# Kernel tuning notes

Measured on AMD Instinct MI355X. Metric: run time of the kernel, lower is better.

Reference implementation:

```python
import jax, jax.numpy as jnp
import numpy as np

BETA = 0.25
SK_EPSILONS = [0.0, 0.0, 0.003]
SK_ITERS = 50
B_SIZE = 262144
LATENT_DIM = 32
K = 256


def setup_inputs() -> dict:
    key = jax.random.key(0)
    kz, k0, k1, k2 = jax.random.split(key, 4)
    return {
        "z": jax.random.normal(kz, (B_SIZE, LATENT_DIM), dtype=jnp.float32),
        "cb0": jax.random.normal(k0, (K, LATENT_DIM), dtype=jnp.float32),
        "cb1": jax.random.normal(k1, (K, LATENT_DIM), dtype=jnp.float32),
        "cb2": jax.random.normal(k2, (K, LATENT_DIM), dtype=jnp.float32),
    }


def _sq_dists(residual, codebook):
    # ||r - c||^2 = ||r||^2 + ||c||^2 - 2 r.c  -> (B, K), avoids (B,K,D) broadcast
    r2 = jnp.sum(residual * residual, axis=1, keepdims=True)      # (B,1)
    c2 = jnp.sum(codebook * codebook, axis=1)                     # (K,)
    cross = residual @ codebook.T                                 # (B,K)
    return r2 + c2 - 2.0 * cross


def _sinkhorn(d_centered, epsilon, n_iters):
    # log-domain Sinkhorn-Knopp, matches torch reference
    B, Kk = d_centered.shape
    log_B = jnp.log(jnp.asarray(B, dtype=d_centered.dtype))
    log_K = jnp.log(jnp.asarray(Kk, dtype=d_centered.dtype))
    log_Q = -d_centered / epsilon
    log_Q = log_Q - jax.scipy.special.logsumexp(log_Q)

    def body(_, lq):
        lq = lq - jax.scipy.special.logsumexp(lq, axis=1, keepdims=True) - log_B
        lq = lq - jax.scipy.special.logsumexp(lq, axis=0, keepdims=True) - log_K
        return lq

    log_Q = jax.lax.fori_loop(0, n_iters, body, log_Q)
    return jnp.exp(log_Q + log_B)


def _quantize_level(residual, codebook, sk_epsilon, use_sk=True):
    dists = _sq_dists(residual, codebook)  # (B, K)
    codes_argmin = jnp.argmin(dists, axis=-1)
    if use_sk and sk_epsilon > 0:
        d = jax.lax.stop_gradient(dists)
        d_max = jnp.max(d)
        d_min = jnp.min(d)
        mid = (d_max + d_min) / 2
        amp = jnp.maximum(d_max - mid, 1e-05)
        Q = _sinkhorn((d - mid) / amp, sk_epsilon, SK_ITERS)
        bad = jnp.any(jnp.isnan(Q)) | jnp.any(jnp.isinf(Q))
        codes = jnp.where(bad, codes_argmin, jnp.argmax(Q, axis=-1))
    else:
        codes = codes_argmin
    quantized = codebook[codes]  # (B, D) gather
    return codes, quantized


def reference(z, cb0, cb1, cb2):
    codebooks = [cb0, cb1, cb2]
    sg = jax.lax.stop_gradient
    residual = z
    all_codes = []
    quantized_total = jnp.zeros_like(z)
    rq_loss = jnp.asarray(0.0, dtype=z.dtype)
    for codebook, sk_epsilon in zip(codebooks, SK_EPSILONS):
        codes, e = _quantize_level(residual, codebook, sk_epsilon, use_sk=True)
        all_codes.append(codes)
        rq_loss = rq_loss + jnp.mean((sg(residual) - e) ** 2)
        rq_loss = rq_loss + BETA * jnp.mean((residual - sg(e)) ** 2)
        e_st = residual + sg(e - residual)  # straight-through
        quantized_total = quantized_total + e_st
        residual = residual - sg(e)
    return (all_codes[0], all_codes[1], all_codes[2], quantized_total, rq_loss)
```

## Files before the change

kernel.cpp:

```cpp
#include <hip/hip_runtime.h>


#define BSZ   262144
#define DIM   32
#define KK    256
#define CHUNK 128
#define NBLK  (BSZ / CHUNK)
#define ITBLK 256
#define NIBLK (BSZ / ITBLK)
#define LROW  36
#define SKEPS 0.003f
#define NIT   50

#define WS_SSQ  0
#define WS_MINK 1
#define WS_MAXK 2
#define WS_TWOT 3
#define WS_W0   256
#define WS_WA   512
#define WS_SIGB 4096
#define WS_BHU  8192
#define WS_BLU  12288

#define OC0   0
#define OC1   BSZ
#define OC2   (2 * BSZ)
#define OQ    (3 * BSZ)
#define OLOSS (3 * BSZ + BSZ * DIM)
#define OU_AH (3u * BSZ)
#define OU_AL (3u * BSZ + 4194304u)

typedef _Float16 half8 __attribute__((ext_vector_type(8)));
typedef float f32x4 __attribute__((ext_vector_type(4)));

#if __has_builtin(__builtin_amdgcn_exp2f)
#define EXP2(x) __builtin_amdgcn_exp2f(x)
#else
#define EXP2(x) exp2f(x)
#endif

#if __has_builtin(__builtin_amdgcn_update_dpp)
#define ROR16(x, N)                                                            \
  __int_as_float(__builtin_amdgcn_update_dpp(__float_as_int(x),                \
                 __float_as_int(x), 0x120 + (N), 0xF, 0xF, false))
#else
#define ROR16(x, N) __shfl_xor((x), (N))
#endif

__device__ __forceinline__ float wred_max(float x) {
  x = fmaxf(x, ROR16(x, 1)); x = fmaxf(x, ROR16(x, 2));
  x = fmaxf(x, ROR16(x, 4)); x = fmaxf(x, ROR16(x, 8));
  x = fmaxf(x, __shfl_xor(x, 16)); x = fmaxf(x, __shfl_xor(x, 32));
  return x;
}
__device__ __forceinline__ float wred_min(float x) {
  x = fminf(x, ROR16(x, 1)); x = fminf(x, ROR16(x, 2));
  x = fminf(x, ROR16(x, 4)); x = fminf(x, ROR16(x, 8));
  x = fminf(x, __shfl_xor(x, 16)); x = fminf(x, __shfl_xor(x, 32));
  return x;
}
__device__ __forceinline__ float wred_sum(float x) {
  x += ROR16(x, 1); x += ROR16(x, 2); x += ROR16(x, 4); x += ROR16(x, 8);
  x += __shfl_xor(x, 16); x += __shfl_xor(x, 32);
  return x;
}
__device__ __forceinline__ float g16_max(float x) {
  x = fmaxf(x, ROR16(x, 1)); x = fmaxf(x, ROR16(x, 2));
  x = fmaxf(x, ROR16(x, 4)); x = fmaxf(x, ROR16(x, 8));
  return x;
}
__device__ __forceinline__ float g16_sum(float x) {
  x += ROR16(x, 1); x += ROR16(x, 2); x += ROR16(x, 4); x += ROR16(x, 8);
  return x;
}

__device__ __forceinline__ unsigned fkey(float f) {
  unsigned b = __float_as_uint(f);
  return (b & 0x80000000u) ? ~b : (b | 0x80000000u);
}
__device__ __forceinline__ float fkeyinv(unsigned k) {
  return __uint_as_float((k & 0x80000000u) ? (k ^ 0x80000000u) : ~k);
}
__device__ __forceinline__ unsigned pk2h(_Float16 a, _Float16 b) {
  unsigned short ua = __builtin_bit_cast(unsigned short, a);
  unsigned short ub = __builtin_bit_cast(unsigned short, b);
  return (unsigned)ua | ((unsigned)ub << 16);
}

__device__ __forceinline__ void load_cbregs_pin(const float* __restrict__ cb, int lane,
                                                float scale, float cbr[4][DIM]) {
#pragma unroll
  for (int c = 0; c < 4; ++c) {
    const float4* p = reinterpret_cast<const float4*>(cb + (4 * lane + c) * DIM);
#pragma unroll
    for (int k = 0; k < 8; ++k) {
      float4 v = p[k];
      cbr[c][4 * k + 0] = v.x * scale; cbr[c][4 * k + 1] = v.y * scale;
      cbr[c][4 * k + 2] = v.z * scale; cbr[c][4 * k + 3] = v.w * scale;
    }
  }
}
__device__ __forceinline__ void cb_norms(const float cbr[4][DIM], float c2[4]) {
#pragma unroll
  for (int c = 0; c < 4; ++c) {
    float s = 0.f;
#pragma unroll
    for (int i = 0; i < DIM; ++i) s = fmaf(cbr[c][i], cbr[c][i], s);
    c2[c] = s;
  }
}
__device__ __forceinline__ void dot4x4(const float* zr, const float cbr[4][DIM],
                                       float v[4][4]) {
#pragma unroll
  for (int d = 0; d < DIM; d += 4) {
#pragma unroll
    for (int q = 0; q < 4; ++q) {
      float4 a = *reinterpret_cast<const float4*>(zr + q * LROW + d);
#pragma unroll
      for (int c = 0; c < 4; ++c) {
        v[q][c] = fmaf(cbr[c][d + 0], a.x, v[q][c]);
        v[q][c] = fmaf(cbr[c][d + 1], a.y, v[q][c]);
        v[q][c] = fmaf(cbr[c][d + 2], a.z, v[q][c]);
        v[q][c] = fmaf(cbr[c][d + 3], a.w, v[q][c]);
      }
    }
  }
}

__global__ void init_k(unsigned* __restrict__ wsu, unsigned long long* __restrict__ sig0) {
  sig0[threadIdx.x] = 0ull;
  if (threadIdx.x == 0) {
    wsu[WS_SSQ] = 0u; wsu[WS_MINK] = 0xFFFFFFFFu; wsu[WS_MAXK] = 0u;
  }
}

__device__ __forceinline__ void argmin_phase(const float* __restrict__ cb, const float* zl,
                                             const float* rsq, int* codel, int lane, int wid) {
  float cbr[4][DIM], c2[4];
  load_cbregs_pin(cb, lane, 1.0f, cbr);
  cb_norms(cbr, c2);
  for (int rb = 0; rb < 8; ++rb) {
    const int r0 = wid * 32 + rb * 4;
    float v[4][4];
#pragma unroll
    for (int q = 0; q < 4; ++q) { v[q][0] = 0.f; v[q][1] = 0.f; v[q][2] = 0.f; v[q][3] = 0.f; }
    dot4x4(&zl[r0 * LROW], cbr, v);
    float d0[4], d1[4], d2[4], d3[4], bq[4], mq[4];
#pragma unroll
    for (int q = 0; q < 4; ++q) {
      float r2 = rsq[r0 + q];
      d0[q] = fmaf(-2.f, v[q][0], r2 + c2[0]);
      d1[q] = fmaf(-2.f, v[q][1], r2 + c2[1]);
      d2[q] = fmaf(-2.f, v[q][2], r2 + c2[2]);
      d3[q] = fmaf(-2.f, v[q][3], r2 + c2[3]);
      bq[q] = fminf(fminf(d0[q], d1[q]), fminf(d2[q], d3[q]));
    }
#pragma unroll
    for (int q = 0; q < 4; ++q) mq[q] = wred_min(bq[q]);
#pragma unroll
    for (int q = 0; q < 4; ++q) {
      int cbi = (d0[q] == mq[q]) ? 0 : ((d1[q] == mq[q]) ? 1 : ((d2[q] == mq[q]) ? 2 : 3));
      unsigned long long bl = __ballot(bq[q] == mq[q]);
      int src = __ffsll(bl) - 1;
      int code = __shfl(4 * lane + cbi, src);
      if (lane == 0) codel[r0 + q] = code;
    }
  }
}

__device__ __forceinline__ void remap_phase(const float* __restrict__ cb, float* zl,
                                            float* rsq, const int* codel, int tid) {
  int row = tid & (CHUNK - 1);
  int half = tid >> 7;
  const float4* cbg = reinterpret_cast<const float4*>(cb + codel[row] * DIM + half * 16);
  float4* zr = reinterpret_cast<float4*>(&zl[row * LROW + half * 16]);
  float local = 0.f;
#pragma unroll
  for (int k = 0; k < 4; ++k) {
    float4 cv = cbg[k];
    float4 v = zr[k];
    v.x -= cv.x; v.y -= cv.y; v.z -= cv.z; v.w -= cv.w;
    zr[k] = v;
    local = fmaf(v.x, v.x, local); local = fmaf(v.y, v.y, local);
    local = fmaf(v.z, v.z, local); local = fmaf(v.w, v.w, local);
  }
  atomicAdd(&rsq[row], local);
}

__global__ __launch_bounds__(256, 2) void stageA_k(const float* __restrict__ z,
                                                   const float* __restrict__ cb0,
                                                   const float* __restrict__ cb1,
                                                   const float* __restrict__ cb2,
                                                   float* __restrict__ out,
                                                   unsigned* __restrict__ outu,
                                                   unsigned* __restrict__ wsu,
                                                   float* __restrict__ wsf) {
  __shared__ float zl[CHUNK * LROW];
  __shared__ float rsq[CHUNK];
  __shared__ int codel[CHUNK];
  __shared__ float red[4];
  const int tid = threadIdx.x, lane = tid & 63, wid = tid >> 6;
  const long base = (long)blockIdx.x * CHUNK;

#pragma unroll
  for (int g = 0; g < 4; ++g) {
    int f4 = g * 256 + tid;
    float4 v = reinterpret_cast<const float4*>(z + base * DIM)[f4];
    int row = f4 >> 3, d = (f4 & 7) * 4;
    *reinterpret_cast<float4*>(&zl[row * LROW + d]) = v;
  }
  __syncthreads();
  if (tid < CHUNK) {
    float s = 0.f;
#pragma unroll
    for (int d = 0; d < DIM; ++d) { float x = zl[tid * LROW + d]; s = fmaf(x, x, s); }
    rsq[tid] = s;
  }
  __syncthreads();

  float loss_acc = 0.f;

  argmin_phase(cb0, zl, rsq, codel, lane, wid);
  __syncthreads();
  if (tid < CHUNK) { out[OC0 + base + tid] = (float)codel[tid]; rsq[tid] = 0.f; }
  __syncthreads();
  remap_phase(cb0, zl, rsq, codel, tid);
  __syncthreads();
  if (tid < CHUNK) loss_acc += rsq[tid];

  argmin_phase(cb1, zl, rsq, codel, lane, wid);
  __syncthreads();
  if (tid < CHUNK) { out[OC1 + base + tid] = (float)codel[tid]; rsq[tid] = 0.f; }
  __syncthreads();
  remap_phase(cb1, zl, rsq, codel, tid);
  __syncthreads();
  if (tid < CHUNK) loss_acc += rsq[tid];

#pragma unroll
  for (int g2 = 0; g2 < 8; ++g2) {
    int slot = g2 * 256 + tid;
    int b = slot >> 8;
    int l = (slot >> 2) & 63;
    int u = slot & 3;
    int row = b * 16 + (l & 15);
    int k = (l >> 4) * 8 + u * 2;
    float x0 = zl[row * LROW + k], x1 = zl[row * LROW + k + 1];
    _Float16 h0 = (_Float16)x0, h1 = (_Float16)x1;
    _Float16 q0 = (_Float16)(x0 - (float)h0), q1 = (_Float16)(x1 - (float)h1);
    unsigned gbase = ((unsigned)blockIdx.x * 8u + (unsigned)b) * 256u + (unsigned)(l * 4 + u);
    outu[OU_AH + gbase] = pk2h(h0, h1);
    outu[OU_AL + gbase] = pk2h(q0, q1);
  }

  {
    float cbr[4][DIM], c2[4];
    load_cbregs_pin(cb2, lane, 1.0f, cbr);
    cb_norms(cbr, c2);
    float dmn = 3.4e38f, dmx = -3.4e38f;
    for (int rb = 0; rb < 8; ++rb) {
      const int r0 = wid * 32 + rb * 4;
      float v[4][4];
#pragma unroll
      for (int q = 0; q < 4; ++q) { v[q][0] = 0.f; v[q][1] = 0.f; v[q][2] = 0.f; v[q][3] = 0.f; }
      dot4x4(&zl[r0 * LROW], cbr, v);
#pragma unroll
      for (int q = 0; q < 4; ++q) {
        float r2 = rsq[r0 + q];
#pragma unroll
        for (int c = 0; c < 4; ++c) {
          float dd = fmaf(-2.f, v[q][c], r2 + c2[c]);
          dmn = fminf(dmn, dd); dmx = fmaxf(dmx, dd);
        }
      }
    }
    dmn = wred_min(dmn);
    dmx = wred_max(dmx);
    if (lane == 0) {
      atomicMin(&wsu[WS_MINK], fkey(dmn));
      atomicMax(&wsu[WS_MAXK], fkey(dmx));
    }
  }

  loss_acc = wred_sum(loss_acc);
  if (lane == 0) red[wid] = loss_acc;
  __syncthreads();
  if (tid == 0) atomicAdd(&wsf[WS_SSQ], red[0] + red[1] + red[2] + red[3]);
}

__global__ void prep_k(const float* __restrict__ cb2, unsigned* __restrict__ wsu,
                       float* __restrict__ wsf, unsigned* __restrict__ bh,
                       unsigned* __restrict__ bl) {
  int j = threadIdx.x;
  float dmin = fkeyinv(wsu[WS_MINK]);
  float dmax = fkeyinv(wsu[WS_MAXK]);
  float mid = (dmax + dmin) * 0.5f;
  float amp = fmaxf(dmax - mid, 1e-5f);
  float t = 1.0f / (amp * SKEPS);
  const float L2E = 1.4426950408889634f;
  float T2L = 2.0f * t * L2E;
  if (j == 0) wsf[WS_TWOT] = T2L;
  float s = 0.f;
#pragma unroll
  for (int d = 0; d < DIM; ++d) { float c = cb2[j * DIM + d]; s = fmaf(c, c, s); }
  wsf[WS_W0 + j] = -t * L2E * s;
  for (int g = 0; g < 16; ++g) {
    int slot = g * 256 + j;
    int jt = slot >> 8, l = (slot >> 2) & 63, u = slot & 3;
    int col = jt * 16 + (l & 15);
    int k = (l >> 4) * 8 + u * 2;
    float b0 = T2L * cb2[col * DIM + k], b1 = T2L * cb2[col * DIM + k + 1];
    _Float16 h0 = (_Float16)b0, h1 = (_Float16)b1;
    _Float16 q0 = (_Float16)(b0 - (float)h0), q1 = (_Float16)(b1 - (float)h1);
    bh[slot] = pk2h(h0, h1);
    bl[slot] = pk2h(q0, q1);
  }
}

__global__ __launch_bounds__(256, 2) void iter_k(const uint4* __restrict__ afh,
                                                 const uint4* __restrict__ afl,
                                                 const uint4* __restrict__ bfh,
                                                 const uint4* __restrict__ bfl,
                                                 const float* __restrict__ w_rd,
                                                 float* __restrict__ w_wr,
                                                 const unsigned long long* __restrict__ s_rd,
                                                 unsigned long long* __restrict__ s_wr,
                                                 unsigned long long* __restrict__ s_zr,
                                                 int first) {
  __shared__ float wsh[KK];
  __shared__ float exm[8][2][2][16];
  __shared__ float exs[8][2][2][16];
  __shared__ float ssh[2][KK];
  const int tid = threadIdx.x, lane = tid & 63, wv = tid >> 6;
  const int pair = wv >> 1, ch = wv & 1, g = lane >> 4;

  {
    float wj = first ? w_rd[tid]
                     : w_rd[tid] + 34.0f - log2f(fmaxf((float)s_rd[tid], 1.0f));
    wsh[tid] = wj;
    if (blockIdx.x == 0) { w_wr[tid] = wj; s_zr[tid] = 0ull; }
  }
  half8 Bh[8], Bl[8];
#pragma unroll
  for (int jt = 0; jt < 8; ++jt) {
    Bh[jt] = __builtin_bit_cast(half8, bfh[(ch * 8 + jt) * 64 + lane]);
    Bl[jt] = __builtin_bit_cast(half8, bfl[(ch * 8 + jt) * 64 + lane]);
  }
  __syncthreads();
  float wc[8];
#pragma unroll
  for (int jt = 0; jt < 8; ++jt) wc[jt] = wsh[(ch * 8 + jt) * 16 + (lane & 15)];

  float sg[8] = {0.f, 0.f, 0.f, 0.f, 0.f, 0.f, 0.f, 0.f};

  for (int b = 0; b < 8; ++b) {
    const int batchid = blockIdx.x * 16 + pair * 8 + b;
    half8 Ah = __builtin_bit_cast(half8, afh[batchid * 64 + lane]);
    half8 Al = __builtin_bit_cast(half8, afl[batchid * 64 + lane]);
    f32x4 v[8];
#pragma unroll
    for (int jt = 0; jt < 8; ++jt) {
      f32x4 acc = {0.f, 0.f, 0.f, 0.f};
      acc = __builtin_amdgcn_mfma_f32_16x16x32_f16(Al, Bl[jt], acc, 0, 0, 0);
      acc = __builtin_amdgcn_mfma_f32_16x16x32_f16(Al, Bh[jt], acc, 0, 0, 0);
      acc = __builtin_amdgcn_mfma_f32_16x16x32_f16(Ah, Bl[jt], acc, 0, 0, 0);
      acc = __builtin_amdgcn_mfma_f32_16x16x32_f16(Ah, Bh[jt], acc, 0, 0, 0);
      v[jt] = acc;
    }
    float m[4];
#pragma unroll
    for (int r = 0; r < 4; ++r) {
#pragma unroll
      for (int jt = 0; jt < 8; ++jt) v[jt][r] += wc[jt];
      float a01 = fmaxf(v[0][r], v[1][r]), a23 = fmaxf(v[2][r], v[3][r]);
      float a45 = fmaxf(v[4][r], v[5][r]), a67 = fmaxf(v[6][r], v[7][r]);
      m[r] = g16_max(fmaxf(fmaxf(a01, a23), fmaxf(a45, a67)));
    }
    float s[4];
#pragma unroll
    for (int r = 0; r < 4; ++r) {
#pragma unroll
      for (int jt = 0; jt < 8; ++jt) v[jt][r] = EXP2(v[jt][r] - m[r]);
      float s01 = v[0][r] + v[1][r], s23 = v[2][r] + v[3][r];
      float s45 = v[4][r] + v[5][r], s67 = v[6][r] + v[7][r];
      s[r] = g16_sum((s01 + s23) + (s45 + s67));
    }
    if ((lane & 15) == 0) {
      *reinterpret_cast<float4*>(&exm[b][pair][ch][g * 4]) = make_float4(m[0], m[1], m[2], m[3]);
      *reinterpret_cast<float4*>(&exs[b][pair][ch][g * 4]) = make_float4(s[0], s[1], s[2], s[3]);
    }
    __syncthreads();
    float4 pm = *reinterpret_cast<const float4*>(&exm[b][pair][ch ^ 1][g * 4]);
    float4 ps = *reinterpret_cast<const float4*>(&exs[b][pair][ch ^ 1][g * 4]);
    float rinv[4];
    {
      float pmv[4] = {pm.x, pm.y, pm.z, pm.w};
      float psv[4] = {ps.x, ps.y, ps.z, ps.w};
#pragma unroll
      for (int r = 0; r < 4; ++r) {
        float M = fmaxf(m[r], pmv[r]);
        float sc = EXP2(m[r] - M);
        float tot = fmaf(s[r], sc, psv[r] * EXP2(pmv[r] - M));
        rinv[r] = sc * __builtin_amdgcn_rcpf(tot);
      }
    }
#pragma unroll
    for (int jt = 0; jt < 8; ++jt)
#pragma unroll
      for (int r = 0; r < 4; ++r) sg[jt] = fmaf(v[jt][r], rinv[r], sg[jt]);
  }
#pragma unroll
  for (int jt = 0; jt < 8; ++jt) {
    float x = sg[jt];
    x += __shfl_xor(x, 16); x += __shfl_xor(x, 32);
    sg[jt] = x;
  }
  if (lane < 16) {
#pragma unroll
    for (int jt = 0; jt < 8; ++jt) ssh[pair][ch * 128 + jt * 16 + lane] = sg[jt];
  }
  __syncthreads();
  float stot = ssh[0][tid] + ssh[1][tid];
  atomicAdd(&s_wr[tid], (unsigned long long)fmaf(stot, 16777216.0f, 0.5f));
}

__global__ __launch_bounds__(256, 2) void final_k(const float* __restrict__ z,
                                                  const float* __restrict__ cb0,
                                                  const float* __restrict__ cb1,
                                                  const float* __restrict__ cb2,
                                                  float* __restrict__ out,
                                                  const float* __restrict__ wsf,
                                                  float* __restrict__ wssq,
                                                  const float* __restrict__ w_rd,
                                                  const unsigned long long* __restrict__ s_rd) {
  __shared__ float zl[CHUNK * LROW];
  __shared__ float wsh[KK];
  __shared__ int codel[CHUNK];
  __shared__ float red[4];
  const int tid = threadIdx.x, lane = tid & 63, wid = tid >> 6;
  const long base = (long)blockIdx.x * CHUNK;

  wsh[tid] = w_rd[tid] + 34.0f - log2f(fmaxf((float)s_rd[tid], 1.0f));

#pragma unroll
  for (int g = 0; g < 4; ++g) {
    int f4 = g * 256 + tid;
    float4 vv = reinterpret_cast<const float4*>(z + base * DIM)[f4];
    int row = f4 >> 3, d = (f4 & 7) * 4;
    *reinterpret_cast<float4*>(&zl[row * LROW + d]) = vv;
  }
  __syncthreads();
  {
    int row = tid & (CHUNK - 1);
    int half = tid >> 7;
    int c0 = (int)out[OC0 + base + row];
    int c1 = (int)out[OC1 + base + row];
    const float4* e0 = reinterpret_cast<const float4*>(cb0 + c0 * DIM + half * 16);
    const float4* e1 = reinterpret_cast<const float4*>(cb1 + c1 * DIM + half * 16);
    float4* zr = reinterpret_cast<float4*>(&zl[row * LROW + half * 16]);
#pragma unroll
    for (int k = 0; k < 4; ++k) {
      float4 a = e0[k], bb = e1[k], v = zr[k];
      v.x = (v.x - a.x) - bb.x; v.y = (v.y - a.y) - bb.y;
      v.z = (v.z - a.z) - bb.z; v.w = (v.w - a.w) - bb.w;
      zr[k] = v;
    }
  }
  const float twot = wsf[WS_TWOT];
  float cbr[4][DIM];
  load_cbregs_pin(cb2, lane, twot, cbr);
  __syncthreads();
  float wc[4];
#pragma unroll
  for (int c = 0; c < 4; ++c) wc[c] = wsh[4 * lane + c];

  for (int rb = 0; rb < 8; ++rb) {
    const int r0 = wid * 32 + rb * 4;
    float v[4][4];
#pragma unroll
    for (int q = 0; q < 4; ++q) { v[q][0] = wc[0]; v[q][1] = wc[1]; v[q][2] = wc[2]; v[q][3] = wc[3]; }
    dot4x4(&zl[r0 * LROW], cbr, v);
    float bq[4], mq[4];
#pragma unroll
    for (int q = 0; q < 4; ++q)
      bq[q] = fmaxf(fmaxf(v[q][0], v[q][1]), fmaxf(v[q][2], v[q][3]));
#pragma unroll
    for (int q = 0; q < 4; ++q) mq[q] = wred_max(bq[q]);
#pragma unroll
    for (int q = 0; q < 4; ++q) {
      int cbi = (v[q][0] == mq[q]) ? 0 : ((v[q][1] == mq[q]) ? 1 : ((v[q][2] == mq[q]) ? 2 : 3));
      unsigned long long bl = __ballot(bq[q] == mq[q]);
      int src = __ffsll(bl) - 1;
      int code = __shfl(4 * lane + cbi, src);
      if (lane == 0) codel[r0 + q] = code;
    }
  }
  __syncthreads();
  if (tid < CHUNK) out[OC2 + base + tid] = (float)codel[tid];
  float loss_acc = 0.f;
#pragma unroll
  for (int g = 0; g < 4; ++g) {
    int f4 = g * 256 + tid;
    int row = f4 >> 3, d = (f4 & 7) * 4;
    float4 e = *reinterpret_cast<const float4*>(cb2 + codel[row] * DIM + d);
    float4 r = *reinterpret_cast<const float4*>(&zl[row * LROW + d]);
    float4 zv = reinterpret_cast<const float4*>(z + base * DIM)[f4];
    float4 q;
    q.x = zv.x - r.x + e.x; q.y = zv.y - r.y + e.y;
    q.z = zv.z - r.z + e.z; q.w = zv.w - r.w + e.w;
    reinterpret_cast<float4*>(out + OQ + base * DIM)[f4] = q;
    float rx = r.x - e.x, ry = r.y - e.y, rz = r.z - e.z, rw = r.w - e.w;
    loss_acc = fmaf(rx, rx, loss_acc); loss_acc = fmaf(ry, ry, loss_acc);
    loss_acc = fmaf(rz, rz, loss_acc); loss_acc = fmaf(rw, rw, loss_acc);
  }
  loss_acc = wred_sum(loss_acc);
  if (lane == 0) red[wid] = loss_acc;
  __syncthreads();
  if (tid == 0) atomicAdd(&wssq[WS_SSQ], red[0] + red[1] + red[2] + red[3]);
}

__global__ void losswrite_k(float* __restrict__ out, const float* __restrict__ wsf) {
  if (threadIdx.x == 0) out[OLOSS] = 1.25f * wsf[WS_SSQ] / 8388608.0f;
}

extern "C" void kernel_launch(void* const* d_in, const int* in_sizes, int n_in,
                              void* d_out, int out_size, void* d_ws, size_t ws_size,
                              hipStream_t stream) {
  const float* z   = (const float*)d_in[0];
  const float* cb0 = (const float*)d_in[1];
  const float* cb1 = (const float*)d_in[2];
  const float* cb2 = (const float*)d_in[3];
  float* out = (float*)d_out;
  unsigned* outu = (unsigned*)d_out;
  float* wsf = (float*)d_ws;
  unsigned* wsu = (unsigned*)d_ws;
  unsigned long long* sig = (unsigned long long*)((char*)d_ws + WS_SIGB);
  unsigned* bh = (unsigned*)d_ws + WS_BHU;
  unsigned* bl = (unsigned*)d_ws + WS_BLU;

  const uint4* afh = (const uint4*)(outu + OU_AH);
  const uint4* afl = (const uint4*)(outu + OU_AL);
  const uint4* bfh = (const uint4*)bh;
  const uint4* bfl = (const uint4*)bl;

  init_k<<<1, 256, 0, stream>>>(wsu, sig);
  stageA_k<<<NBLK, 256, 0, stream>>>(z, cb0, cb1, cb2, out, outu, wsu, wsf);
  prep_k<<<1, 256, 0, stream>>>(cb2, wsu, wsf, bh, bl);
  for (int it = 0; it < NIT; ++it) {
    const float* w_rd = (it == 0) ? (wsf + WS_W0) : (wsf + WS_WA + ((it - 1) & 1) * KK);
    float* w_wr = wsf + WS_WA + (it & 1) * KK;
    const unsigned long long* s_rd = sig + KK * ((it + 2) % 3);
    unsigned long long* s_wr = sig + KK * (it % 3);
    unsigned long long* s_zr = sig + KK * ((it + 1) % 3);
    iter_k<<<NIBLK, 256, 0, stream>>>(afh, afl, bfh, bfl, w_rd, w_wr, s_rd, s_wr, s_zr,
                                      it == 0 ? 1 : 0);
  }
  final_k<<<NBLK, 256, 0, stream>>>(z, cb0, cb1, cb2, out, wsf, wsf,
                                    wsf + WS_WA + ((NIT - 1) & 1) * KK,
                                    sig + KK * ((NIT - 1) % 3));
  losswrite_k<<<1, 64, 0, stream>>>(out, wsf);
}
```

Baseline: 2.334 ms.

## Move distance GEMMs to bf16x3 MFMA and split final stage into codes/output kernels

Replaces the scalar FMA dot-product loops for the level-0/1 argmin, the level-2 min/max scan and the final Sinkhorn argmax with MFMA 16x16x32 bf16 instructions. Inputs are split into three bf16 terms and combined with six MFMAs to keep near-fp32 accuracy, using codebook fragments precomputed in a new prep kernel. The iteration kernel is restructured, and the final stage is split into a code-selection kernel and a separate kernel that rebuilds the quantized output and loss from the stored codes. The gain is tensor-core throughput; the costs are the extra split arithmetic, possible argmax tie or rounding differences, and re-reading z and the codes in the new output pass.

```diff
diff --git a/kernel.cpp b/kernel.cpp
--- a/kernel.cpp
+++ b/kernel.cpp
@@ -6,8 +6,7 @@
 #define KK    256
 #define CHUNK 128
 #define NBLK  (BSZ / CHUNK)
-#define ITBLK 256
-#define NIBLK (BSZ / ITBLK)
+#define NIBLK (BSZ / 256)
 #define LROW  36
 #define SKEPS 0.003f
 #define NIT   50
@@ -18,9 +17,11 @@
 #define WS_TWOT 3
 #define WS_W0   256
 #define WS_WA   512
-#define WS_SIGB 4096
-#define WS_BHU  8192
-#define WS_BLU  12288
+#define WS_C2   1024
+#define WSB_SIG 8192
+#define WSB_BH  16384
+#define WSB_BL  32768
+#define WSB_QB  49152
 
 #define OC0   0
 #define OC1   BSZ
@@ -30,6 +31,7 @@
 #define OU_AH (3u * BSZ)
 #define OU_AL (3u * BSZ + 4194304u)
 
+typedef short short8 __attribute__((ext_vector_type(8)));
 typedef _Float16 half8 __attribute__((ext_vector_type(8)));
 typedef float f32x4 __attribute__((ext_vector_type(4)));
 
@@ -43,8 +45,10 @@
 #define ROR16(x, N)                                                            \
   __int_as_float(__builtin_amdgcn_update_dpp(__float_as_int(x),                \
                  __float_as_int(x), 0x120 + (N), 0xF, 0xF, false))
+#define ROR16I(x, N) __builtin_amdgcn_update_dpp((x), (x), 0x120 + (N), 0xF, 0xF, false)
 #else
 #define ROR16(x, N) __shfl_xor((x), (N))
+#define ROR16I(x, N) __shfl_xor((x), (N))
 #endif
 
 __device__ __forceinline__ float wred_max(float x) {
@@ -73,6 +77,12 @@
   x += ROR16(x, 1); x += ROR16(x, 2); x += ROR16(x, 4); x += ROR16(x, 8);
   return x;
 }
+__device__ __forceinline__ void g16_argmax(float& v, int& j) {
+  { float ov = ROR16(v,1); int oj = ROR16I(j,1); if (ov > v || (ov == v && oj < j)) { v = ov; j = oj; } }
+  { float ov = ROR16(v,2); int oj = ROR16I(j,2); if (ov > v || (ov == v && oj < j)) { v = ov; j = oj; } }
+  { float ov = ROR16(v,4); int oj = ROR16I(j,4); if (ov > v || (ov == v && oj < j)) { v = ov; j = oj; } }
+  { float ov = ROR16(v,8); int oj = ROR16I(j,8); if (ov > v || (ov == v && oj < j)) { v = ov; j = oj; } }
+}
 
 __device__ __forceinline__ unsigned fkey(float f) {
   unsigned b = __float_as_uint(f);
@@ -86,90 +96,115 @@
   unsigned short ub = __builtin_bit_cast(unsigned short, b);
   return (unsigned)ua | ((unsigned)ub << 16);
 }
-
-__device__ __forceinline__ void load_cbregs_pin(const float* __restrict__ cb, int lane,
-                                                float scale, float cbr[4][DIM]) {
-#pragma unroll
-  for (int c = 0; c < 4; ++c) {
-    const float4* p = reinterpret_cast<const float4*>(cb + (4 * lane + c) * DIM);
-#pragma unroll
-    for (int k = 0; k < 8; ++k) {
-      float4 v = p[k];
-      cbr[c][4 * k + 0] = v.x * scale; cbr[c][4 * k + 1] = v.y * scale;
-      cbr[c][4 * k + 2] = v.z * scale; cbr[c][4 * k + 3] = v.w * scale;
-    }
-  }
-}
-__device__ __forceinline__ void cb_norms(const float cbr[4][DIM], float c2[4]) {
-#pragma unroll
-  for (int c = 0; c < 4; ++c) {
+__device__ __forceinline__ unsigned short bf16rne(float x) {
+  unsigned u = __float_as_uint(x);
+  return (unsigned short)((u + 0x7FFFu + ((u >> 16) & 1u)) >> 16);
+}
+__device__ __forceinline__ float bf2f(unsigned short h) {
+  return __uint_as_float(((unsigned)h) << 16);
+}
+__device__ __forceinline__ void split3_8(const float* xs, short8& a1, short8& a2, short8& a3) {
+#pragma unroll
+  for (int u = 0; u < 8; ++u) {
+    float x = xs[u];
+    unsigned short b1 = bf16rne(x); x -= bf2f(b1);
+    unsigned short b2 = bf16rne(x); x -= bf2f(b2);
+    unsigned short b3 = bf16rne(x);
+    a1[u] = (short)b1; a2[u] = (short)b2; a3[u] = (short)b3;
+  }
+}
+__device__ __forceinline__ f32x4 mfma6(short8 A1, short8 A2, short8 A3,
+                                       const uint4* __restrict__ q1,
+                                       const uint4* __restrict__ q2,
+                                       const uint4* __restrict__ q3,
+                                       int idx, f32x4 acc) {
+  short8 B1 = __builtin_bit_cast(short8, q1[idx]);
+  short8 B2 = __builtin_bit_cast(short8, q2[idx]);
+  short8 B3 = __builtin_bit_cast(short8, q3[idx]);
+  acc = __builtin_amdgcn_mfma_f32_16x16x32_bf16(A3, B1, acc, 0, 0, 0);
+  acc = __builtin_amdgcn_mfma_f32_16x16x32_bf16(A1, B3, acc, 0, 0, 0);
+  acc = __builtin_amdgcn_mfma_f32_16x16x32_bf16(A2, B2, acc, 0, 0, 0);
+  acc = __builtin_amdgcn_mfma_f32_16x16x32_bf16(A2, B1, acc, 0, 0, 0);
+  acc = __builtin_amdgcn_mfma_f32_16x16x32_bf16(A1, B2, acc, 0, 0, 0);
+  acc = __builtin_amdgcn_mfma_f32_16x16x32_bf16(A1, B1, acc, 0, 0, 0);
+  return acc;
+}
+__device__ __forceinline__ void build_a(const float* zl, int b, int lane,
+                                        short8& A1, short8& A2, short8& A3) {
+  int row = b * 16 + (lane & 15);
+  int kb = (lane >> 4) * 8;
+  float xs[8];
+  float4 t0 = *reinterpret_cast<const float4*>(&zl[row * LROW + kb]);
+  float4 t1 = *reinterpret_cast<const float4*>(&zl[row * LROW + kb + 4]);
+  xs[0]=t0.x; xs[1]=t0.y; xs[2]=t0.z; xs[3]=t0.w;
+  xs[4]=t1.x; xs[5]=t1.y; xs[6]=t1.z; xs[7]=t1.w;
+  split3_8(xs, A1, A2, A3);
+}
+
+__global__ void prep0_k(const float* __restrict__ cb0, const float* __restrict__ cb1,
+                        const float* __restrict__ cb2, unsigned* __restrict__ wsu,
+                        float* __restrict__ wsf, uint4* __restrict__ qb,
+                        unsigned long long* __restrict__ sig0) {
+  int t = threadIdx.x;
+  sig0[t] = 0ull;
+  if (t == 0) { wsu[WS_SSQ] = 0u; wsu[WS_MINK] = 0xFFFFFFFFu; wsu[WS_MAXK] = 0u; }
+  const float* cbs[3] = {cb0, cb1, cb2};
+  for (int lvl = 0; lvl < 3; ++lvl) {
+    const float* cb = cbs[lvl];
     float s = 0.f;
 #pragma unroll
-    for (int i = 0; i < DIM; ++i) s = fmaf(cbr[c][i], cbr[c][i], s);
-    c2[c] = s;
-  }
-}
-__device__ __forceinline__ void dot4x4(const float* zr, const float cbr[4][DIM],
-                                       float v[4][4]) {
-#pragma unroll
-  for (int d = 0; d < DIM; d += 4) {
-#pragma unroll
-    for (int q = 0; q < 4; ++q) {
-      float4 a = *reinterpret_cast<const float4*>(zr + q * LROW + d);
-#pragma unroll
-      for (int c = 0; c < 4; ++c) {
-        v[q][c] = fmaf(cbr[c][d + 0], a.x, v[q][c]);
-        v[q][c] = fmaf(cbr[c][d + 1], a.y, v[q][c]);
-        v[q][c] = fmaf(cbr[c][d + 2], a.z, v[q][c]);
-        v[q][c] = fmaf(cbr[c][d + 3], a.w, v[q][c]);
-      }
-    }
-  }
-}
-
-__global__ void init_k(unsigned* __restrict__ wsu, unsigned long long* __restrict__ sig0) {
-  sig0[threadIdx.x] = 0ull;
-  if (threadIdx.x == 0) {
-    wsu[WS_SSQ] = 0u; wsu[WS_MINK] = 0xFFFFFFFFu; wsu[WS_MAXK] = 0u;
-  }
-}
-
-__device__ __forceinline__ void argmin_phase(const float* __restrict__ cb, const float* zl,
-                                             const float* rsq, int* codel, int lane, int wid) {
-  float cbr[4][DIM], c2[4];
-  load_cbregs_pin(cb, lane, 1.0f, cbr);
-  cb_norms(cbr, c2);
-  for (int rb = 0; rb < 8; ++rb) {
-    const int r0 = wid * 32 + rb * 4;
-    float v[4][4];
-#pragma unroll
-    for (int q = 0; q < 4; ++q) { v[q][0] = 0.f; v[q][1] = 0.f; v[q][2] = 0.f; v[q][3] = 0.f; }
-    dot4x4(&zl[r0 * LROW], cbr, v);
-    float d0[4], d1[4], d2[4], d3[4], bq[4], mq[4];
-#pragma unroll
-    for (int q = 0; q < 4; ++q) {
-      float r2 = rsq[r0 + q];
-      d0[q] = fmaf(-2.f, v[q][0], r2 + c2[0]);
-      d1[q] = fmaf(-2.f, v[q][1], r2 + c2[1]);
-      d2[q] = fmaf(-2.f, v[q][2], r2 + c2[2]);
-      d3[q] = fmaf(-2.f, v[q][3], r2 + c2[3]);
-      bq[q] = fminf(fminf(d0[q], d1[q]), fminf(d2[q], d3[q]));
-    }
-#pragma unroll
-    for (int q = 0; q < 4; ++q) mq[q] = wred_min(bq[q]);
-#pragma unroll
-    for (int q = 0; q < 4; ++q) {
-      int cbi = (d0[q] == mq[q]) ? 0 : ((d1[q] == mq[q]) ? 1 : ((d2[q] == mq[q]) ? 2 : 3));
-      unsigned long long bl = __ballot(bq[q] == mq[q]);
-      int src = __ffsll(bl) - 1;
-      int code = __shfl(4 * lane + cbi, src);
-      if (lane == 0) codel[r0 + q] = code;
-    }
-  }
-}
-
-__device__ __forceinline__ void remap_phase(const float* __restrict__ cb, float* zl,
-                                            float* rsq, const int* codel, int tid) {
+    for (int d = 0; d < DIM; ++d) { float c = cb[t * DIM + d]; s = fmaf(c, c, s); }
+    wsf[WS_C2 + lvl * 256 + t] = 0.5f * s;
+    for (int g = 0; g < 4; ++g) {
+      int slot = g * 256 + t;
+      int jt = slot >> 6, l = slot & 63;
+      int col = jt * 16 + (l & 15), kb = (l >> 4) * 8;
+      float xs[8];
+#pragma unroll
+      for (int u = 0; u < 8; ++u) xs[u] = cb[col * DIM + kb + u];
+      short8 b1, b2, b3;
+      split3_8(xs, b1, b2, b3);
+      qb[(lvl * 3 + 0) * 1024 + slot] = __builtin_bit_cast(uint4, b1);
+      qb[(lvl * 3 + 1) * 1024 + slot] = __builtin_bit_cast(uint4, b2);
+      qb[(lvl * 3 + 2) * 1024 + slot] = __builtin_bit_cast(uint4, b3);
+    }
+  }
+}
+
+__device__ __forceinline__ void argmin_mfma(const uint4* __restrict__ q1,
+                                            const uint4* __restrict__ q2,
+                                            const uint4* __restrict__ q3,
+                                            const float* __restrict__ c2p,
+                                            const float* zl, int* codel,
+                                            int lane, int wid) {
+  float c2h[16];
+#pragma unroll
+  for (int jt = 0; jt < 16; ++jt) c2h[jt] = c2p[jt * 16 + (lane & 15)];
+  for (int bb = 0; bb < 2; ++bb) {
+    int b = wid * 2 + bb;
+    short8 A1, A2, A3;
+    build_a(zl, b, lane, A1, A2, A3);
+    float bv[4] = {-3.4e38f, -3.4e38f, -3.4e38f, -3.4e38f};
+    int bj[4] = {0, 0, 0, 0};
+    for (int jt = 0; jt < 16; ++jt) {
+      f32x4 acc = {-c2h[jt], -c2h[jt], -c2h[jt], -c2h[jt]};
+      acc = mfma6(A1, A2, A3, q1, q2, q3, jt * 64 + lane, acc);
+      int col = jt * 16 + (lane & 15);
+#pragma unroll
+      for (int r = 0; r < 4; ++r)
+        if (acc[r] > bv[r]) { bv[r] = acc[r]; bj[r] = col; }
+    }
+#pragma unroll
+    for (int r = 0; r < 4; ++r) g16_argmax(bv[r], bj[r]);
+    if ((lane & 15) == 0) {
+#pragma unroll
+      for (int r = 0; r < 4; ++r) codel[b * 16 + (lane >> 4) * 4 + r] = bj[r];
+    }
+  }
+}
+
+__device__ __forceinline__ float remap_phase(const float* __restrict__ cb, float* zl,
+                                             const int* codel, int tid) {
   int row = tid & (CHUNK - 1);
   int half = tid >> 7;
   const float4* cbg = reinterpret_cast<const float4*>(cb + codel[row] * DIM + half * 16);
@@ -184,17 +219,17 @@
     local = fmaf(v.x, v.x, local); local = fmaf(v.y, v.y, local);
     local = fmaf(v.z, v.z, local); local = fmaf(v.w, v.w, local);
   }
-  atomicAdd(&rsq[row], local);
+  return local;
 }
 
 __global__ __launch_bounds__(256, 2) void stageA_k(const float* __restrict__ z,
                                                    const float* __restrict__ cb0,
                                                    const float* __restrict__ cb1,
-                                                   const float* __restrict__ cb2,
                                                    float* __restrict__ out,
                                                    unsigned* __restrict__ outu,
                                                    unsigned* __restrict__ wsu,
-                                                   float* __restrict__ wsf) {
+                                                   float* __restrict__ wsf,
+                                                   const uint4* __restrict__ qb) {
   __shared__ float zl[CHUNK * LROW];
   __shared__ float rsq[CHUNK];
   __shared__ int codel[CHUNK];
@@ -210,6 +245,21 @@
     *reinterpret_cast<float4*>(&zl[row * LROW + d]) = v;
   }
   __syncthreads();
+
+  float loss_acc = 0.f;
+
+  argmin_mfma(qb + 0 * 1024, qb + 1 * 1024, qb + 2 * 1024, wsf + WS_C2, zl, codel, lane, wid);
+  __syncthreads();
+  if (tid < CHUNK) out[OC0 + base + tid] = (float)codel[tid];
+  loss_acc += remap_phase(cb0, zl, codel, tid);
+  __syncthreads();
+
+  argmin_mfma(qb + 3 * 1024, qb + 4 * 1024, qb + 5 * 1024, wsf + WS_C2 + 256, zl, codel, lane, wid);
+  __syncthreads();
+  if (tid < CHUNK) out[OC1 + base + tid] = (float)codel[tid];
+  loss_acc += remap_phase(cb1, zl, codel, tid);
+  __syncthreads();
+
   if (tid < CHUNK) {
     float s = 0.f;
 #pragma unroll
@@ -218,23 +268,41 @@
   }
   __syncthreads();
 
-  float loss_acc = 0.f;
-
-  argmin_phase(cb0, zl, rsq, codel, lane, wid);
-  __syncthreads();
-  if (tid < CHUNK) { out[OC0 + base + tid] = (float)codel[tid]; rsq[tid] = 0.f; }
-  __syncthreads();
-  remap_phase(cb0, zl, rsq, codel, tid);
-  __syncthreads();
-  if (tid < CHUNK) loss_acc += rsq[tid];
-
-  argmin_phase(cb1, zl, rsq, codel, lane, wid);
-  __syncthreads();
-  if (tid < CHUNK) { out[OC1 + base + tid] = (float)codel[tid]; rsq[tid] = 0.f; }
-  __syncthreads();
-  remap_phase(cb1, zl, rsq, codel, tid);
-  __syncthreads();
-  if (tid < CHUNK) loss_acc += rsq[tid];
+  {
+    const uint4* q1 = qb + 6 * 1024;
+    const uint4* q2 = qb + 7 * 1024;
+    const uint4* q3 = qb + 8 * 1024;
+    const float* c2p = wsf + WS_C2 + 512;
+    float c2h[16];
+#pragma unroll
+    for (int jt = 0; jt < 16; ++jt) c2h[jt] = c2p[jt * 16 + (lane & 15)];
+    float dmn = 3.4e38f, dmx = -3.4e38f;
+    for (int bb = 0; bb < 2; ++bb) {
+      int b = wid * 2 + bb;
+      short8 A1, A2, A3;
+      build_a(zl, b, lane, A1, A2, A3);
+      float mn[4] = {3.4e38f, 3.4e38f, 3.4e38f, 3.4e38f};
+      float mx[4] = {-3.4e38f, -3.4e38f, -3.4e38f, -3.4e38f};
+      for (int jt = 0; jt < 16; ++jt) {
+        f32x4 acc = {-c2h[jt], -c2h[jt], -c2h[jt], -c2h[jt]};
+        acc = mfma6(A1, A2, A3, q1, q2, q3, jt * 64 + lane, acc);
+#pragma unroll
+        for (int r = 0; r < 4; ++r) { mn[r] = fminf(mn[r], acc[r]); mx[r] = fmaxf(mx[r], acc[r]); }
+      }
+#pragma unroll
+      for (int r = 0; r < 4; ++r) {
+        float r2 = rsq[b * 16 + (lane >> 4) * 4 + r];
+        dmn = fminf(dmn, fmaf(-2.f, mx[r], r2));
+        dmx = fmaxf(dmx, fmaf(-2.f, mn[r], r2));
+      }
+    }
+    dmn = wred_min(dmn);
+    dmx = wred_max(dmx);
+    if (lane == 0) {
+      atomicMin(&wsu[WS_MINK], fkey(dmn));
+      atomicMax(&wsu[WS_MAXK], fkey(dmx));
+    }
+  }
 
 #pragma unroll
   for (int g2 = 0; g2 < 8; ++g2) {
@@ -252,35 +320,6 @@
     outu[OU_AL + gbase] = pk2h(q0, q1);
   }
 
-  {
-    float cbr[4][DIM], c2[4];
-    load_cbregs_pin(cb2, lane, 1.0f, cbr);
-    cb_norms(cbr, c2);
-    float dmn = 3.4e38f, dmx = -3.4e38f;
-    for (int rb = 0; rb < 8; ++rb) {
-      const int r0 = wid * 32 + rb * 4;
-      float v[4][4];
-#pragma unroll
-      for (int q = 0; q < 4; ++q) { v[q][0] = 0.f; v[q][1] = 0.f; v[q][2] = 0.f; v[q][3] = 0.f; }
-      dot4x4(&zl[r0 * LROW], cbr, v);
-#pragma unroll
-      for (int q = 0; q < 4; ++q) {
-        float r2 = rsq[r0 + q];
-#pragma unroll
-        for (int c = 0; c < 4; ++c) {
-          float dd = fmaf(-2.f, v[q][c], r2 + c2[c]);
-          dmn = fminf(dmn, dd); dmx = fmaxf(dmx, dd);
-        }
-      }
-    }
-    dmn = wred_min(dmn);
-    dmx = wred_max(dmx);
-    if (lane == 0) {
-      atomicMin(&wsu[WS_MINK], fkey(dmn));
-      atomicMax(&wsu[WS_MAXK], fkey(dmx));
-    }
-  }
-
   loss_acc = wred_sum(loss_acc);
   if (lane == 0) red[wid] = loss_acc;
   __syncthreads();
@@ -289,7 +328,7 @@
 
 __global__ void prep_k(const float* __restrict__ cb2, unsigned* __restrict__ wsu,
                        float* __restrict__ wsf, unsigned* __restrict__ bh,
-                       unsigned* __restrict__ bl) {
+                       unsigned* __restrict__ bl, uint4* __restrict__ qb) {
   int j = threadIdx.x;
   float dmin = fkeyinv(wsu[WS_MINK]);
   float dmax = fkeyinv(wsu[WS_MAXK]);
@@ -314,6 +353,19 @@
     bh[slot] = pk2h(h0, h1);
     bl[slot] = pk2h(q0, q1);
   }
+  for (int g = 0; g < 4; ++g) {
+    int slot = g * 256 + j;
+    int jt = slot >> 6, l = slot & 63;
+    int col = jt * 16 + (l & 15), kb = (l >> 4) * 8;
+    float xs[8];
+#pragma unroll
+    for (int u = 0; u < 8; ++u) xs[u] = T2L * cb2[col * DIM + kb + u];
+    short8 b1v, b2v, b3v;
+    split3_8(xs, b1v, b2v, b3v);
+    qb[9 * 1024 + slot]  = __builtin_bit_cast(uint4, b1v);
+    qb[10 * 1024 + slot] = __builtin_bit_cast(uint4, b2v);
+    qb[11 * 1024 + slot] = __builtin_bit_cast(uint4, b3v);
+  }
 }
 
 __global__ __launch_bounds__(256, 2) void iter_k(const uint4* __restrict__ afh,
@@ -327,11 +379,8 @@
                                                  unsigned long long* __restrict__ s_zr,
                                                  int first) {
   __shared__ float wsh[KK];
-  __shared__ float exm[8][2][2][16];
-  __shared__ float exs[8][2][2][16];
-  __shared__ float ssh[2][KK];
+  __shared__ float ssh[4][KK];
   const int tid = threadIdx.x, lane = tid & 63, wv = tid >> 6;
-  const int pair = wv >> 1, ch = wv & 1, g = lane >> 4;
 
   {
     float wj = first ? w_rd[tid]
@@ -339,114 +388,124 @@
     wsh[tid] = wj;
     if (blockIdx.x == 0) { w_wr[tid] = wj; s_zr[tid] = 0ull; }
   }
-  half8 Bh[8], Bl[8];
-#pragma unroll
-  for (int jt = 0; jt < 8; ++jt) {
-    Bh[jt] = __builtin_bit_cast(half8, bfh[(ch * 8 + jt) * 64 + lane]);
-    Bl[jt] = __builtin_bit_cast(half8, bfl[(ch * 8 + jt) * 64 + lane]);
-  }
-  __syncthreads();
-  float wc[8];
-#pragma unroll
-  for (int jt = 0; jt < 8; ++jt) wc[jt] = wsh[(ch * 8 + jt) * 16 + (lane & 15)];
-
-  float sg[8] = {0.f, 0.f, 0.f, 0.f, 0.f, 0.f, 0.f, 0.f};
-
-  for (int b = 0; b < 8; ++b) {
-    const int batchid = blockIdx.x * 16 + pair * 8 + b;
+  __syncthreads();
+  float wc[16];
+#pragma unroll
+  for (int jt = 0; jt < 16; ++jt) wc[jt] = wsh[jt * 16 + (lane & 15)];
+
+  float sg[16];
+#pragma unroll
+  for (int jt = 0; jt < 16; ++jt) sg[jt] = 0.f;
+
+  for (int bb = 0; bb < 4; ++bb) {
+    const int batchid = blockIdx.x * 16 + wv * 4 + bb;
     half8 Ah = __builtin_bit_cast(half8, afh[batchid * 64 + lane]);
     half8 Al = __builtin_bit_cast(half8, afl[batchid * 64 + lane]);
-    f32x4 v[8];
-#pragma unroll
-    for (int jt = 0; jt < 8; ++jt) {
+    f32x4 p1[8], p2[8];
+    float m1[4], s1[4], m2[4], s2[4];
+#pragma unroll
+    for (int j = 0; j < 8; ++j) {
+      half8 Bh = __builtin_bit_cast(half8, bfh[j * 64 + lane]);
+      half8 Bl = __builtin_bit_cast(half8, bfl[j * 64 + lane]);
       f32x4 acc = {0.f, 0.f, 0.f, 0.f};
-      acc = __builtin_amdgcn_mfma_f32_16x16x32_f16(Al, Bl[jt], acc, 0, 0, 0);
-      acc = __builtin_amdgcn_mfma_f32_16x16x32_f16(Al, Bh[jt], acc, 0, 0, 0);
-      acc = __builtin_amdgcn_mfma_f32_16x16x32_f16(Ah, Bl[jt], acc, 0, 0, 0);
-      acc = __builtin_amdgcn_mfma_f32_16x16x32_f16(Ah, Bh[jt], acc, 0, 0, 0);
-      v[jt] = acc;
-    }
-    float m[4];
+      acc = __builtin_amdgcn_mfma_f32_16x16x32_f16(Al, Bl, acc, 0, 0, 0);
+      acc = __builtin_amdgcn_mfma_f32_16x16x32_f16(Al, Bh, acc, 0, 0, 0);
+      acc = __builtin_amdgcn_mfma_f32_16x16x32_f16(Ah, Bl, acc, 0, 0, 0);
+      acc = __builtin_amdgcn_mfma_f32_16x16x32_f16(Ah, Bh, acc, 0, 0, 0);
+#pragma unroll
+      for (int r = 0; r < 4; ++r) acc[r] += wc[j];
+      p1[j] = acc;
+    }
 #pragma unroll
     for (int r = 0; r < 4; ++r) {
-#pragma unroll
-      for (int jt = 0; jt < 8; ++jt) v[jt][r] += wc[jt];
-      float a01 = fmaxf(v[0][r], v[1][r]), a23 = fmaxf(v[2][r], v[3][r]);
-      float a45 = fmaxf(v[4][r], v[5][r]), a67 = fmaxf(v[6][r], v[7][r]);
-      m[r] = g16_max(fmaxf(fmaxf(a01, a23), fmaxf(a45, a67)));
-    }
-    float s[4];
+      float a = fmaxf(fmaxf(p1[0][r], p1[1][r]), fmaxf(p1[2][r], p1[3][r]));
+      float b = fmaxf(fmaxf(p1[4][r], p1[5][r]), fmaxf(p1[6][r], p1[7][r]));
+      m1[r] = g16_max(fmaxf(a, b));
+    }
 #pragma unroll
     for (int r = 0; r < 4; ++r) {
 #pragma unroll
-      for (int jt = 0; jt < 8; ++jt) v[jt][r] = EXP2(v[jt][r] - m[r]);
-      float s01 = v[0][r] + v[1][r], s23 = v[2][r] + v[3][r];
-      float s45 = v[4][r] + v[5][r], s67 = v[6][r] + v[7][r];
-      s[r] = g16_sum((s01 + s23) + (s45 + s67));
-    }
-    if ((lane & 15) == 0) {
-      *reinterpret_cast<float4*>(&exm[b][pair][ch][g * 4]) = make_float4(m[0], m[1], m[2], m[3]);
-      *reinterpret_cast<float4*>(&exs[b][pair][ch][g * 4]) = make_float4(s[0], s[1], s[2], s[3]);
-    }
-    __syncthreads();
-    float4 pm = *reinterpret_cast<const float4*>(&exm[b][pair][ch ^ 1][g * 4]);
-    float4 ps = *reinterpret_cast<const float4*>(&exs[b][pair][ch ^ 1][g * 4]);
-    float rinv[4];
-    {
-      float pmv[4] = {pm.x, pm.y, pm.z, pm.w};
-      float psv[4] = {ps.x, ps.y, ps.z, ps.w};
-#pragma unroll
-      for (int r = 0; r < 4; ++r) {
-        float M = fmaxf(m[r], pmv[r]);
-        float sc = EXP2(m[r] - M);
-        float tot = fmaf(s[r], sc, psv[r] * EXP2(pmv[r] - M));
-        rinv[r] = sc * __builtin_amdgcn_rcpf(tot);
+      for (int j = 0; j < 8; ++j) p1[j][r] = EXP2(p1[j][r] - m1[r]);
+      float a = (p1[0][r] + p1[1][r]) + (p1[2][r] + p1[3][r]);
+      float b = (p1[4][r] + p1[5][r]) + (p1[6][r] + p1[7][r]);
+      s1[r] = g16_sum(a + b);
+    }
+#pragma unroll
+    for (int j = 0; j < 8; ++j) {
+      half8 Bh = __builtin_bit_cast(half8, bfh[(8 + j) * 64 + lane]);
+      half8 Bl = __builtin_bit_cast(half8, bfl[(8 + j) * 64 + lane]);
+      f32x4 acc = {0.f, 0.f, 0.f, 0.f};
+      acc = __builtin_amdgcn_mfma_f32_16x16x32_f16(Al, Bl, acc, 0, 0, 0);
+      acc = __builtin_amdgcn_mfma_f32_16x16x32_f16(Al, Bh, acc, 0, 0, 0);
+      acc = __builtin_amdgcn_mfma_f32_16x16x32_f16(Ah, Bl, acc, 0, 0, 0);
+      acc = __builtin_amdgcn_mfma_f32_16x16x32_f16(Ah, Bh, acc, 0, 0, 0);
+#pragma unroll
+      for (int r = 0; r < 4; ++r) acc[r] += wc[8 + j];
+      p2[j] = acc;
+    }
+#pragma unroll
+    for (int r = 0; r < 4; ++r) {
+      float a = fmaxf(fmaxf(p2[0][r], p2[1][r]), fmaxf(p2[2][r], p2[3][r]));
+      float b = fmaxf(fmaxf(p2[4][r], p2[5][r]), fmaxf(p2[6][r], p2[7][r]));
+      m2[r] = g16_max(fmaxf(a, b));
+    }
+#pragma unroll
+    for (int r = 0; r < 4; ++r) {
+#pragma unroll
+      for (int j = 0; j < 8; ++j) p2[j][r] = EXP2(p2[j][r] - m2[r]);
+      float a = (p2[0][r] + p2[1][r]) + (p2[2][r] + p2[3][r]);
+      float b = (p2[4][r] + p2[5][r]) + (p2[6][r] + p2[7][r]);
+      s2[r] = g16_sum(a + b);
+    }
+#pragma unroll
+    for (int r = 0; r < 4; ++r) {
+      float M = fmaxf(m1[r], m2[r]);
+      float f1 = EXP2(m1[r] - M), f2 = EXP2(m2[r] - M);
+      float tot = fmaf(s1[r], f1, s2[r] * f2);
+      float it = __builtin_amdgcn_rcpf(tot);
+      float r1 = f1 * it, r2v = f2 * it;
+#pragma unroll
+      for (int j = 0; j < 8; ++j) {
+        sg[j]     = fmaf(p1[j][r], r1,  sg[j]);
+        sg[8 + j] = fmaf(p2[j][r], r2v, sg[8 + j]);
       }
     }
-#pragma unroll
-    for (int jt = 0; jt < 8; ++jt)
-#pragma unroll
-      for (int r = 0; r < 4; ++r) sg[jt] = fmaf(v[jt][r], rinv[r], sg[jt]);
-  }
-#pragma unroll
-  for (int jt = 0; jt < 8; ++jt) {
+  }
+#pragma unroll
+  for (int jt = 0; jt < 16; ++jt) {
     float x = sg[jt];
     x += __shfl_xor(x, 16); x += __shfl_xor(x, 32);
     sg[jt] = x;
   }
   if (lane < 16) {
 #pragma unroll
-    for (int jt = 0; jt < 8; ++jt) ssh[pair][ch * 128 + jt * 16 + lane] = sg[jt];
-  }
-  __syncthreads();
-  float stot = ssh[0][tid] + ssh[1][tid];
-  atomicAdd(&s_wr[tid], (unsigned long long)fmaf(stot, 16777216.0f, 0.5f));
-}
-
-__global__ __launch_bounds__(256, 2) void final_k(const float* __restrict__ z,
-                                                  const float* __restrict__ cb0,
-                                                  const float* __restrict__ cb1,
-                                                  const float* __restrict__ cb2,
-                                                  float* __restrict__ out,
-                                                  const float* __restrict__ wsf,
-                                                  float* __restrict__ wssq,
-                                                  const float* __restrict__ w_rd,
-                                                  const unsigned long long* __restrict__ s_rd) {
+    for (int jt = 0; jt < 16; ++jt) ssh[wv][jt * 16 + lane] = sg[jt];
+  }
+  __syncthreads();
+  float s = ssh[0][tid] + ssh[1][tid] + ssh[2][tid] + ssh[3][tid];
+  atomicAdd(&s_wr[tid], (unsigned long long)fmaf(s, 16777216.0f, 0.5f));
+}
+
+__global__ __launch_bounds__(256, 2) void fcodes_k(const float* __restrict__ z,
+                                                   const float* __restrict__ cb0,
+                                                   const float* __restrict__ cb1,
+                                                   float* __restrict__ out,
+                                                   const uint4* __restrict__ qb,
+                                                   const float* __restrict__ w_rd,
+                                                   const unsigned long long* __restrict__ s_rd) {
   __shared__ float zl[CHUNK * LROW];
   __shared__ float wsh[KK];
   __shared__ int codel[CHUNK];
-  __shared__ float red[4];
   const int tid = threadIdx.x, lane = tid & 63, wid = tid >> 6;
   const long base = (long)blockIdx.x * CHUNK;
 
   wsh[tid] = w_rd[tid] + 34.0f - log2f(fmaxf((float)s_rd[tid], 1.0f));
-
 #pragma unroll
   for (int g = 0; g < 4; ++g) {
     int f4 = g * 256 + tid;
-    float4 vv = reinterpret_cast<const float4*>(z + base * DIM)[f4];
+    float4 v = reinterpret_cast<const float4*>(z + base * DIM)[f4];
     int row = f4 >> 3, d = (f4 & 7) * 4;
-    *reinterpret_cast<float4*>(&zl[row * LROW + d]) = vv;
+    *reinterpret_cast<float4*>(&zl[row * LROW + d]) = v;
   }
   __syncthreads();
   {
@@ -465,57 +524,78 @@
       zr[k] = v;
     }
   }
-  const float twot = wsf[WS_TWOT];
-  float cbr[4][DIM];
-  load_cbregs_pin(cb2, lane, twot, cbr);
-  __syncthreads();
-  float wc[4];
-#pragma unroll
-  for (int c = 0; c < 4; ++c) wc[c] = wsh[4 * lane + c];
-
-  for (int rb = 0; rb < 8; ++rb) {
-    const int r0 = wid * 32 + rb * 4;
-    float v[4][4];
-#pragma unroll
-    for (int q = 0; q < 4; ++q) { v[q][0] = wc[0]; v[q][1] = wc[1]; v[q][2] = wc[2]; v[q][3] = wc[3]; }
-    dot4x4(&zl[r0 * LROW], cbr, v);
-    float bq[4], mq[4];
-#pragma unroll
-    for (int q = 0; q < 4; ++q)
-      bq[q] = fmaxf(fmaxf(v[q][0], v[q][1]), fmaxf(v[q][2], v[q][3]));
-#pragma unroll
-    for (int q = 0; q < 4; ++q) mq[q] = wred_max(bq[q]);
-#pragma unroll
-    for (int q = 0; q < 4; ++q) {
-      int cbi = (v[q][0] == mq[q]) ? 0 : ((v[q][1] == mq[q]) ? 1 : ((v[q][2] == mq[q]) ? 2 : 3));
-      unsigned long long bl = __ballot(bq[q] == mq[q]);
-      int src = __ffsll(bl) - 1;
-      int code = __shfl(4 * lane + cbi, src);
-      if (lane == 0) codel[r0 + q] = code;
+  __syncthreads();
+
+  const uint4* q1 = qb + 9 * 1024;
+  const uint4* q2 = qb + 10 * 1024;
+  const uint4* q3 = qb + 11 * 1024;
+  float wc[16];
+#pragma unroll
+  for (int jt = 0; jt < 16; ++jt) wc[jt] = wsh[jt * 16 + (lane & 15)];
+  for (int bb = 0; bb < 2; ++bb) {
+    int b = wid * 2 + bb;
+    short8 A1, A2, A3;
+    build_a(zl, b, lane, A1, A2, A3);
+    float bv[4] = {-3.4e38f, -3.4e38f, -3.4e38f, -3.4e38f};
+    int bj[4] = {0, 0, 0, 0};
+    for (int jt = 0; jt < 16; ++jt) {
+      f32x4 acc = {wc[jt], wc[jt], wc[jt], wc[jt]};
+      acc = mfma6(A1, A2, A3, q1, q2, q3, jt * 64 + lane, acc);
+      int col = jt * 16 + (lane & 15);
+#pragma unroll
+      for (int r = 0; r < 4; ++r)
+        if (acc[r] > bv[r]) { bv[r] = acc[r]; bj[r] = col; }
+    }
+#pragma unroll
+    for (int r = 0; r < 4; ++r) g16_argmax(bv[r], bj[r]);
+    if ((lane & 15) == 0) {
+#pragma unroll
+      for (int r = 0; r < 4; ++r) codel[b * 16 + (lane >> 4) * 4 + r] = bj[r];
     }
   }
   __syncthreads();
   if (tid < CHUNK) out[OC2 + base + tid] = (float)codel[tid];
-  float loss_acc = 0.f;
-#pragma unroll
-  for (int g = 0; g < 4; ++g) {
-    int f4 = g * 256 + tid;
-    int row = f4 >> 3, d = (f4 & 7) * 4;
-    float4 e = *reinterpret_cast<const float4*>(cb2 + codel[row] * DIM + d);
-    float4 r = *reinterpret_cast<const float4*>(&zl[row * LROW + d]);
-    float4 zv = reinterpret_cast<const float4*>(z + base * DIM)[f4];
+}
+
+__global__ __launch_bounds__(256) void fout_k(const float* __restrict__ z,
+                                              const float* __restrict__ cb0,
+                                              const float* __restrict__ cb1,
+                                              const float* __restrict__ cb2,
+                                              float* __restrict__ out,
+                                              float* __restrict__ wsf) {
+  __shared__ int cc0[256], cc1[256], cc2[256];
+  __shared__ float red[4];
+  const int tid = threadIdx.x, lane = tid & 63, wv = tid >> 6;
+  const long rbase = (long)blockIdx.x * 256;
+  cc0[tid] = (int)out[OC0 + rbase + tid];
+  cc1[tid] = (int)out[OC1 + rbase + tid];
+  cc2[tid] = (int)out[OC2 + rbase + tid];
+  __syncthreads();
+  float loss = 0.f;
+#pragma unroll
+  for (int g = 0; g < 8; ++g) {
+    long f4 = (long)blockIdx.x * 2048 + g * 256 + tid;
+    int lrow = (g * 256 + tid) >> 3;
+    int d4 = (g * 256 + tid) & 7;
+    float4 zv = reinterpret_cast<const float4*>(z)[f4];
+    float4 e0 = *reinterpret_cast<const float4*>(&cb0[cc0[lrow] * DIM + d4 * 4]);
+    float4 e1 = *reinterpret_cast<const float4*>(&cb1[cc1[lrow] * DIM + d4 * 4]);
+    float4 e2 = *reinterpret_cast<const float4*>(&cb2[cc2[lrow] * DIM + d4 * 4]);
     float4 q;
-    q.x = zv.x - r.x + e.x; q.y = zv.y - r.y + e.y;
-    q.z = zv.z - r.z + e.z; q.w = zv.w - r.w + e.w;
-    reinterpret_cast<float4*>(out + OQ + base * DIM)[f4] = q;
-    float rx = r.x - e.x, ry = r.y - e.y, rz = r.z - e.z, rw = r.w - e.w;
-    loss_acc = fmaf(rx, rx, loss_acc); loss_acc = fmaf(ry, ry, loss_acc);
-    loss_acc = fmaf(rz, rz, loss_acc); loss_acc = fmaf(rw, rw, loss_acc);
-  }
-  loss_acc = wred_sum(loss_acc);
-  if (lane == 0) red[wid] = loss_acc;
-  __syncthreads();
-  if (tid == 0) atomicAdd(&wssq[WS_SSQ], red[0] + red[1] + red[2] + red[3]);
+    q.x = (e0.x + e1.x) + e2.x; q.y = (e0.y + e1.y) + e2.y;
+    q.z = (e0.z + e1.z) + e2.z; q.w = (e0.w + e1.w) + e2.w;
+    reinterpret_cast<float4*>(out + OQ)[f4] = q;
+    float rx = ((zv.x - e0.x) - e1.x) - e2.x;
+    float ry = ((zv.y - e0.y) - e1.y) - e2.y;
+    float rz = ((zv.z - e0.z) - e1.z) - e2.z;
+    float rw = ((zv.w - e0.w) - e1.w) - e2.w;
+    loss = fmaf(rx, rx, loss); loss = fmaf(ry, ry, loss);
+    loss = fmaf(rz, rz, loss); loss = fmaf(rw, rw, loss);
+  }
+  loss = wred_sum(loss);
+  if (lane == 0) red[wv] = loss;
+  __syncthreads();
+  if (tid == 0) atomicAdd(&wsf[WS_SSQ], red[0] + red[1] + red[2] + red[3]);
 }
 
 __global__ void losswrite_k(float* __restrict__ out, const float* __restrict__ wsf) {
@@ -533,18 +613,19 @@
   unsigned* outu = (unsigned*)d_out;
   float* wsf = (float*)d_ws;
   unsigned* wsu = (unsigned*)d_ws;
-  unsigned long long* sig = (unsigned long long*)((char*)d_ws + WS_SIGB);
-  unsigned* bh = (unsigned*)d_ws + WS_BHU;
-  unsigned* bl = (unsigned*)d_ws + WS_BLU;
+  unsigned long long* sig = (unsigned long long*)((char*)d_ws + WSB_SIG);
+  unsigned* bh = (unsigned*)((char*)d_ws + WSB_BH);
+  unsigned* bl = (unsigned*)((char*)d_ws + WSB_BL);
+  uint4* qb = (uint4*)((char*)d_ws + WSB_QB);
 
   const uint4* afh = (const uint4*)(outu + OU_AH);
   const uint4* afl = (const uint4*)(outu + OU_AL);
   const uint4* bfh = (const uint4*)bh;
   const uint4* bfl = (const uint4*)bl;
 
-  init_k<<<1, 256, 0, stream>>>(wsu, sig);
-  stageA_k<<<NBLK, 256, 0, stream>>>(z, cb0, cb1, cb2, out, outu, wsu, wsf);
-  prep_k<<<1, 256, 0, stream>>>(cb2, wsu, wsf, bh, bl);
+  prep0_k<<<1, 256, 0, stream>>>(cb0, cb1, cb2, wsu, wsf, qb, sig);
+  stageA_k<<<NBLK, 256, 0, stream>>>(z, cb0, cb1, out, outu, wsu, wsf, qb);
+  prep_k<<<1, 256, 0, stream>>>(cb2, wsu, wsf, bh, bl, qb);
   for (int it = 0; it < NIT; ++it) {
     const float* w_rd = (it == 0) ? (wsf + WS_W0) : (wsf + WS_WA + ((it - 1) & 1) * KK);
     float* w_wr = wsf + WS_WA + (it & 1) * KK;
@@ -554,8 +635,9 @@
     iter_k<<<NIBLK, 256, 0, stream>>>(afh, afl, bfh, bfl, w_rd, w_wr, s_rd, s_wr, s_zr,
                                       it == 0 ? 1 : 0);
   }
-  final_k<<<NBLK, 256, 0, stream>>>(z, cb0, cb1, cb2, out, wsf, wsf,
-                                    wsf + WS_WA + ((NIT - 1) & 1) * KK,
-                                    sig + KK * ((NIT - 1) % 3));
+  fcodes_k<<<NBLK, 256, 0, stream>>>(z, cb0, cb1, out, qb,
+                                     wsf + WS_WA + ((NIT - 1) & 1) * KK,
+                                     sig + KK * ((NIT - 1) % 3));
+  fout_k<<<NIBLK, 256, 0, stream>>>(z, cb0, cb1, cb2, out, wsf);
   losswrite_k<<<1, 64, 0, stream>>>(out, wsf);
 }
```

Result: slower. 2.515 ms (+7.8%).
